# Performance work log

Hardware: AMD Instinct MI355X
Metric: run time of the kernel (lower is better)

## Reference

```python
import jax, jax.numpy as jnp
import numpy as np

N_HEAD = 16
NEG_BIG = 1e10

def setup_inputs() -> dict:
    key = jax.random.key(0)
    k1, k2, k3 = jax.random.split(key, 3)
    B, S, D = 2, 2048, 1024
    x = jax.random.normal(k1, (B, S, D), dtype=jnp.float32)
    c_attn_w = jax.random.normal(k2, (D, 3 * D), dtype=jnp.float32) * 0.02
    c_attn_b = jnp.zeros((3 * D,), dtype=jnp.float32)
    c_proj_w = jax.random.normal(k3, (D, D), dtype=jnp.float32) * 0.02
    c_proj_b = jnp.zeros((D,), dtype=jnp.float32)
    return {"x": x, "c_attn_w": c_attn_w, "c_attn_b": c_attn_b,
            "c_proj_w": c_proj_w, "c_proj_b": c_proj_b}

def reference(x, c_attn_w, c_attn_b, c_proj_w, c_proj_b):
    B, S, D = x.shape
    H = N_HEAD
    hd = D // H
    # Conv1D c_attn: x @ W + b -> (B, S, 3D)
    qkv = x @ c_attn_w + c_attn_b
    q, k, v = jnp.split(qkv, 3, axis=-1)
    # split heads -> (B, H, S, hd)
    q = q.reshape(B, S, H, hd).transpose(0, 2, 1, 3)
    k = k.reshape(B, S, H, hd).transpose(0, 2, 1, 3)
    v = v.reshape(B, S, H, hd).transpose(0, 2, 1, 3)
    # QK^T with scale (scale=True)
    w = jnp.einsum('bhqd,bhkd->bhqk', q, k) / jnp.sqrt(jnp.float32(hd))
    # additive/multiplicative causal mask, exactly as source: w*b - 1e10*(1-b)
    b = jnp.tril(jnp.ones((S, S), dtype=w.dtype))
    w = w * b - NEG_BIG * (1.0 - b)
    w = jax.nn.softmax(w, axis=-1)
    a = jnp.einsum('bhqk,bhkd->bhqd', w, v)
    # merge heads -> (B, S, D)
    a = a.transpose(0, 2, 1, 3).reshape(B, S, D)
    # Conv1D c_proj
    a = a @ c_proj_w + c_proj_b
    # present = stack(key (as (B,H,S,hd)), value)
    present = jnp.stack((k, v))
    return (a, present)
```

## Files before the change

kernel.cpp:

```cpp
#include <hip/hip_runtime.h>
#include <hip/hip_bf16.h>
#include <string.h>

#define BB 2
#define SS 2048
#define DD 1024
#define NH 16
#define TT (BB * SS)
#define N3 (3 * DD)
#define A_SIZE (TT * DD)
#define PRESENT_HALF (BB * NH * SS * 64)
#define C2Q 0.18033688011112043f

typedef __attribute__((ext_vector_type(8))) short short8;
typedef __attribute__((ext_vector_type(4))) float floatx4;
typedef __attribute__((ext_vector_type(8))) unsigned short ushort8;

__device__ __forceinline__ unsigned short f2bf(float f) {
    union { float f; unsigned u; } v; v.f = f;
    unsigned r = v.u + 0x7fffu + ((v.u >> 16) & 1u);
    return (unsigned short)(r >> 16);
}
__device__ __forceinline__ unsigned pack2bf(float a, float b) {
    __hip_bfloat162 h = __float22bfloat162_rn(float2{a, b});
    unsigned u; memcpy(&u, &h, 4); return u;
}
__device__ __forceinline__ float bf2f(unsigned short u) {
    union { unsigned u; float f; } v; v.u = ((unsigned)u) << 16; return v.f;
}

__device__ __forceinline__ void async16(const unsigned short* g, unsigned short* lds) {
    __builtin_amdgcn_global_load_lds(
        (const __attribute__((address_space(1))) unsigned int*)g,
        (__attribute__((address_space(3))) unsigned int*)lds,
        16, 0, 0);
}

__device__ __forceinline__ void transpose_tile(const float* __restrict__ src,
                                               unsigned short* __restrict__ dst,
                                               int R, int C, int bx, int by, int tid) {
    __shared__ float tile[32][33];
    int c0 = bx * 32, r0 = by * 32;
    int tx = tid & 31, ty = tid >> 5;
    for (int i = ty; i < 32; i += 8)
        tile[i][tx] = src[(size_t)(r0 + i) * C + c0 + tx];
    __syncthreads();
    for (int i = ty; i < 32; i += 8)
        dst[(size_t)(c0 + i) * R + r0 + tx] = f2bf(tile[tx][i]);
}

__global__ __launch_bounds__(256)
void prep_kernel(const float* __restrict__ x,
                 const float* __restrict__ wa,
                 const float* __restrict__ wp,
                 unsigned short* __restrict__ xb,
                 unsigned short* __restrict__ wqkvt,
                 unsigned short* __restrict__ wprojt) {
    int bid = blockIdx.x, tid = threadIdx.x;
    if (bid < 2048) {
        int i = (bid * 256 + tid) * 8;
        float4 a = *(const float4*)(x + i);
        float4 b = *(const float4*)(x + i + 4);
        ushort8 o;
        o[0] = f2bf(a.x); o[1] = f2bf(a.y); o[2] = f2bf(a.z); o[3] = f2bf(a.w);
        o[4] = f2bf(b.x); o[5] = f2bf(b.y); o[6] = f2bf(b.z); o[7] = f2bf(b.w);
        *(ushort8*)(xb + i) = o;
    } else if (bid < 2048 + 3072) {
        int b2 = bid - 2048;
        transpose_tile(wa, wqkvt, DD, N3, b2 % 96, b2 / 96, tid);
    } else {
        int b3 = bid - 5120;
        transpose_tile(wp, wprojt, DD, DD, b3 & 31, b3 >> 5, tid);
    }
}

__global__ __launch_bounds__(256)
void kv_aux_kernel(const unsigned short* __restrict__ qkvb,
                   float* __restrict__ out,
                   unsigned short* __restrict__ vT) {
    __shared__ unsigned short tile[64][72];
    const int bh = blockIdx.x, st = blockIdx.y;
    const int b = bh >> 4, h = bh & 15;
    const int tid = threadIdx.x;
    const int r = tid >> 2, c = (tid & 3) * 16;
    const int s = st * 64 + r;

    const unsigned short* kp = qkvb + ((size_t)(b * SS + s)) * 3072 + 1024 + h * 64 + c;
    ushort8 k0 = *(const ushort8*)(kp);
    ushort8 k1 = *(const ushort8*)(kp + 8);
    ushort8 v0 = *(const ushort8*)(kp + 1024);
    ushort8 v1 = *(const ushort8*)(kp + 1032);

    float* pk = out + A_SIZE + (((size_t)(b * NH + h) * SS + s) * 64 + c);
    *(float4*)(pk)      = float4{bf2f(k0[0]), bf2f(k0[1]), bf2f(k0[2]), bf2f(k0[3])};
    *(float4*)(pk + 4)  = float4{bf2f(k0[4]), bf2f(k0[5]), bf2f(k0[6]), bf2f(k0[7])};
    *(float4*)(pk + 8)  = float4{bf2f(k1[0]), bf2f(k1[1]), bf2f(k1[2]), bf2f(k1[3])};
    *(float4*)(pk + 12) = float4{bf2f(k1[4]), bf2f(k1[5]), bf2f(k1[6]), bf2f(k1[7])};
    float* pv = pk + PRESENT_HALF;
    *(float4*)(pv)      = float4{bf2f(v0[0]), bf2f(v0[1]), bf2f(v0[2]), bf2f(v0[3])};
    *(float4*)(pv + 4)  = float4{bf2f(v0[4]), bf2f(v0[5]), bf2f(v0[6]), bf2f(v0[7])};
    *(float4*)(pv + 8)  = float4{bf2f(v1[0]), bf2f(v1[1]), bf2f(v1[2]), bf2f(v1[3])};
    *(float4*)(pv + 12) = float4{bf2f(v1[4]), bf2f(v1[5]), bf2f(v1[6]), bf2f(v1[7])};

    *(ushort8*)(&tile[r][c])     = v0;
    *(ushort8*)(&tile[r][c + 8]) = v1;
    __syncthreads();
    int d = tid >> 2, s0 = (tid & 3) * 16;
    unsigned short tmp[16];
    for (int e = 0; e < 16; ++e) tmp[e] = tile[s0 + e][d];
    unsigned short* dst = vT + ((size_t)bh * 64 + d) * SS + st * 64 + s0;
    *(int4*)(dst)     = *(const int4*)(tmp);
    *(int4*)(dst + 8) = *(const int4*)(tmp + 8);
}

__global__ __launch_bounds__(256)
void gemm1_kernel(const unsigned short* __restrict__ A,
                  const unsigned short* __restrict__ Bt,
                  const float* __restrict__ bias,
                  unsigned short* __restrict__ out_bf) {
    __shared__ unsigned short As[2][128][32];
    __shared__ unsigned short Bs[2][128][32];
    const int tid  = threadIdx.x;
    const int t0   = blockIdx.y * 128;
    const int n0   = blockIdx.x * 128;
    const int wave = tid >> 6, lane = tid & 63;
    const int wm = wave >> 1, wn = wave & 1;
    const int l15 = lane & 15, quad = lane >> 4;
    const int sr = lane >> 2, sc = (lane & 3) * 8;

    floatx4 acc[4][4];
    for (int i = 0; i < 4; ++i)
        for (int j = 0; j < 4; ++j)
            for (int e = 0; e < 4; ++e) acc[i][j][e] = 0.f;

    const unsigned short* gA = A  + (size_t)(t0 + wave * 32 + sr) * 1024 + sc;
    const unsigned short* gB = Bt + (size_t)(n0 + wave * 32 + sr) * 1024 + sc;

    async16(gA,             &As[0][wave * 32][0]);
    async16(gA + 16 * 1024, &As[0][wave * 32 + 16][0]);
    async16(gB,             &Bs[0][wave * 32][0]);
    async16(gB + 16 * 1024, &Bs[0][wave * 32 + 16][0]);

    for (int kt = 0; kt < 32; ++kt) {
        const int cur = kt & 1;
        __syncthreads();
        if (kt < 31) {
            const int k1 = (kt + 1) * 32;
            async16(gA + k1,             &As[cur ^ 1][wave * 32][0]);
            async16(gA + k1 + 16 * 1024, &As[cur ^ 1][wave * 32 + 16][0]);
            async16(gB + k1,             &Bs[cur ^ 1][wave * 32][0]);
            async16(gB + k1 + 16 * 1024, &Bs[cur ^ 1][wave * 32 + 16][0]);
        }
        short8 af[4], bfr[4];
        for (int mt = 0; mt < 4; ++mt)
            af[mt] = *(const short8*)(&As[cur][wm * 64 + mt * 16 + l15][quad * 8]);
        for (int nt = 0; nt < 4; ++nt)
            bfr[nt] = *(const short8*)(&Bs[cur][wn * 64 + nt * 16 + l15][quad * 8]);
        for (int mt = 0; mt < 4; ++mt)
            for (int nt = 0; nt < 4; ++nt)
                acc[mt][nt] = __builtin_amdgcn_mfma_f32_16x16x32_bf16(bfr[nt], af[mt], acc[mt][nt], 0, 0, 0);
    }

    const float qs = (n0 < 1024) ? C2Q : 1.0f;
    for (int mt = 0; mt < 4; ++mt) {
        const int t = t0 + wm * 64 + mt * 16 + l15;
        unsigned short* po = out_bf + (size_t)t * 3072 + n0 + wn * 64;
        for (int nt = 0; nt < 4; ++nt) {
            float4 b4 = *(const float4*)(bias + n0 + wn * 64 + nt * 16 + quad * 4);
            uint2 w = {pack2bf((acc[mt][nt][0] + b4.x) * qs, (acc[mt][nt][1] + b4.y) * qs),
                       pack2bf((acc[mt][nt][2] + b4.z) * qs, (acc[mt][nt][3] + b4.w) * qs)};
            *(uint2*)(po + nt * 16 + quad * 4) = w;
        }
    }
}

__global__ __launch_bounds__(256)
void gemm2_kernel(const unsigned short* __restrict__ A,
                  const unsigned short* __restrict__ Bt,
                  const float* __restrict__ bias,
                  float* __restrict__ out_f) {
    __shared__ unsigned short As[2][128][32];
    __shared__ unsigned short Bs[2][64][32];
    const int tid  = threadIdx.x;
    const int t0   = blockIdx.y * 128;
    const int n0   = blockIdx.x * 64;
    const int wave = tid >> 6, lane = tid & 63;
    const int wm = wave >> 1, wn = wave & 1;
    const int l15 = lane & 15, quad = lane >> 4;
    const int sr = lane >> 2, sc = (lane & 3) * 8;

    floatx4 acc[4][2];
    for (int i = 0; i < 4; ++i)
        for (int j = 0; j < 2; ++j)
            for (int e = 0; e < 4; ++e) acc[i][j][e] = 0.f;

    const unsigned short* gA = A  + (size_t)(t0 + wave * 32 + sr) * 1024 + sc;
    const unsigned short* gB = Bt + (size_t)(n0 + wave * 16 + sr) * 1024 + sc;

    async16(gA,             &As[0][wave * 32][0]);
    async16(gA + 16 * 1024, &As[0][wave * 32 + 16][0]);
    async16(gB,             &Bs[0][wave * 16][0]);

    for (int kt = 0; kt < 32; ++kt) {
        const int cur = kt & 1;
        __syncthreads();
        if (kt < 31) {
            const int k1 = (kt + 1) * 32;
            async16(gA + k1,             &As[cur ^ 1][wave * 32][0]);
            async16(gA + k1 + 16 * 1024, &As[cur ^ 1][wave * 32 + 16][0]);
            async16(gB + k1,             &Bs[cur ^ 1][wave * 16][0]);
        }
        short8 af[4], bfr[2];
        for (int mt = 0; mt < 4; ++mt)
            af[mt] = *(const short8*)(&As[cur][wm * 64 + mt * 16 + l15][quad * 8]);
        for (int nt = 0; nt < 2; ++nt)
            bfr[nt] = *(const short8*)(&Bs[cur][wn * 32 + nt * 16 + l15][quad * 8]);
        for (int mt = 0; mt < 4; ++mt)
            for (int nt = 0; nt < 2; ++nt)
                acc[mt][nt] = __builtin_amdgcn_mfma_f32_16x16x32_bf16(bfr[nt], af[mt], acc[mt][nt], 0, 0, 0);
    }

    for (int mt = 0; mt < 4; ++mt) {
        const int t = t0 + wm * 64 + mt * 16 + l15;
        float* po = out_f + (size_t)t * 1024 + n0 + wn * 32;
        for (int nt = 0; nt < 2; ++nt) {
            float4 b4 = *(const float4*)(bias + n0 + wn * 32 + nt * 16 + quad * 4);
            float4 v = {acc[mt][nt][0] + b4.x, acc[mt][nt][1] + b4.y,
                        acc[mt][nt][2] + b4.z, acc[mt][nt][3] + b4.w};
            *(float4*)(po + nt * 16 + quad * 4) = v;
        }
    }
}

__global__ __launch_bounds__(512)
void flash_kernel(const unsigned short* __restrict__ qkv,
                  const unsigned short* __restrict__ vT,
                  unsigned short* __restrict__ out) {
    __shared__ unsigned short Kt[2][64][72];
    __shared__ unsigned short Vt[2][64][72];
    __shared__ unsigned short Pt[8][16][72];

    const int bh = blockIdx.x;
    const int yy = blockIdx.y;
    const int qy = (yy & 1) ? (yy >> 1) : (15 - (yy >> 1));
    const int b = bh >> 4, h = bh & 15;
    const int tid = threadIdx.x;
    const int wave = tid >> 6, lane = tid & 63;
    const int group = wave >> 2, w4 = wave & 3;
    const int l15 = lane & 15, quad = lane >> 4;

    const int my_qt = 2 * qy + group;
    const int jmax  = 2 * qy + 1;

    const size_t rowb = (size_t)b * SS;

    short8 bq0, bq1;
    {
        const unsigned short* qp = qkv + (rowb + my_qt * 64 + w4 * 16 + l15) * 3072 + h * 64 + quad * 8;
        bq0 = *(const short8*)(qp);
        bq1 = *(const short8*)(qp + 32);
    }

    float l_i = 0.f;
    floatx4 o[4];
    for (int dt = 0; dt < 4; ++dt)
        for (int e = 0; e < 4; ++e) o[dt][e] = 0.f;

    const int qrow_l = w4 * 16 + l15;

    const int rr = tid >> 3, seg = (tid & 7) * 8;
    const unsigned short* kb = qkv + rowb * 3072 + 1024 + h * 64;
    const unsigned short* vb = vT + (size_t)bh * 64 * SS;
    int4 ka, va;

    #define PREF(j) { ka = *(const int4*)(kb + (size_t)((j) * 64 + rr) * 3072 + seg); \
                      va = *(const int4*)(vb + (size_t)rr * SS + (j) * 64 + seg); }
    #define STAGE(bf_) { *(int4*)(&Kt[bf_][rr][seg]) = ka; *(int4*)(&Vt[bf_][rr][seg]) = va; }

    PREF(0);
    STAGE(0);
    if (jmax > 0) PREF(1);

    for (int j = 0; j <= jmax; ++j) {
        const int cur = j & 1;
        __syncthreads();
        if (j < jmax) {
            STAGE(cur ^ 1);
            if (j + 2 <= jmax) PREF(j + 2);
        }
        if (j > my_qt) continue;

        floatx4 sc[4];
        for (int nt = 0; nt < 4; ++nt)
            for (int e = 0; e < 4; ++e) sc[nt][e] = 0.f;
        for (int nt = 0; nt < 4; ++nt) {
            const unsigned short* kp = &Kt[cur][nt * 16 + l15][quad * 8];
            short8 ak0 = *(const short8*)(kp);
            short8 ak1 = *(const short8*)(kp + 32);
            sc[nt] = __builtin_amdgcn_mfma_f32_16x16x32_bf16(ak0, bq0, sc[nt], 0, 0, 0);
            sc[nt] = __builtin_amdgcn_mfma_f32_16x16x32_bf16(ak1, bq1, sc[nt], 0, 0, 0);
        }
        if (j == my_qt) {
            for (int nt = 0; nt < 4; ++nt)
                for (int r = 0; r < 4; ++r)
                    if (nt * 16 + quad * 4 + r > qrow_l) sc[nt][r] = -1.0e30f;
        }

        for (int nt = 0; nt < 4; ++nt)
            for (int r = 0; r < 4; ++r) {
                float p = __builtin_amdgcn_exp2f(sc[nt][r]);
                sc[nt][r] = p;
                l_i += p;
            }

        for (int nt = 0; nt < 4; ++nt) {
            uint2 w = {pack2bf(sc[nt][0], sc[nt][1]), pack2bf(sc[nt][2], sc[nt][3])};
            *(uint2*)(&Pt[wave][l15][nt * 16 + quad * 4]) = w;
        }
        asm volatile("s_waitcnt lgkmcnt(0)" ::: "memory");
        short8 bp0 = *(const short8*)(&Pt[wave][l15][quad * 8]);
        short8 bp1 = *(const short8*)(&Pt[wave][l15][32 + quad * 8]);
        for (int dt = 0; dt < 4; ++dt) {
            const unsigned short* vp = &Vt[cur][dt * 16 + l15][quad * 8];
            short8 av0 = *(const short8*)(vp);
            short8 av1 = *(const short8*)(vp + 32);
            o[dt] = __builtin_amdgcn_mfma_f32_16x16x32_bf16(av0, bp0, o[dt], 0, 0, 0);
            o[dt] = __builtin_amdgcn_mfma_f32_16x16x32_bf16(av1, bp1, o[dt], 0, 0, 0);
        }
    }
    #undef PREF
    #undef STAGE

    l_i += __shfl_xor(l_i, 16);
    l_i += __shfl_xor(l_i, 32);
    float inv = 1.f / l_i;
    const int qrow = my_qt * 64 + w4 * 16 + l15;
    unsigned short* po = out + (rowb + qrow) * 1024 + h * 64;
    for (int dt = 0; dt < 4; ++dt) {
        uint2 w = {pack2bf(o[dt][0] * inv, o[dt][1] * inv),
                   pack2bf(o[dt][2] * inv, o[dt][3] * inv)};
        *(uint2*)(po + dt * 16 + quad * 4) = w;
    }
}

extern "C" void kernel_launch(void* const* d_in, const int* in_sizes, int n_in,
                              void* d_out, int out_size, void* d_ws, size_t ws_size,
                              hipStream_t stream) {
    const float* x        = (const float*)d_in[0];
    const float* c_attn_w = (const float*)d_in[1];
    const float* c_attn_b = (const float*)d_in[2];
    const float* c_proj_w = (const float*)d_in[3];
    const float* c_proj_b = (const float*)d_in[4];
    float* out = (float*)d_out;

    char* ws = (char*)d_ws;
    unsigned short* xb     = (unsigned short*)(ws);
    unsigned short* wqkvt  = (unsigned short*)(ws + 8388608);
    unsigned short* wprojt = (unsigned short*)(ws + 14680064);
    unsigned short* qkvb   = (unsigned short*)(ws + 16777216);
    unsigned short* aout   = (unsigned short*)(ws + 41943040);
    unsigned short* vT     = xb;

    prep_kernel<<<2048 + 3072 + 1024, 256, 0, stream>>>(x, c_attn_w, c_proj_w, xb, wqkvt, wprojt);
    gemm1_kernel<<<dim3(N3 / 128, TT / 128), 256, 0, stream>>>(xb, wqkvt, c_attn_b, qkvb);
    kv_aux_kernel<<<dim3(32, 32), 256, 0, stream>>>(qkvb, out, vT);
    flash_kernel<<<dim3(32, 16), 512, 0, stream>>>(qkvb, vT, aout);
    gemm2_kernel<<<dim3(DD / 64, TT / 128), 256, 0, stream>>>(aout, wprojt, c_proj_b, out);
}
```

Measured before the change: 219.9 us.

## Load K/V fragments directly from global memory in flash attention, drop LDS staging

The flash kernel no longer stages K and V tiles in shared memory with double buffering and block-wide barriers. Each wave now loads its MFMA operand fragments for K and V straight from global memory (relying on L2/cache reuse). The block shrinks from 512 to 256 threads, each block owns one 64-row query tile, and the grid grows to 32x32 with a new balanced tile ordering. This removes __syncthreads and LDS traffic and allows higher occupancy, at the cost of redundant global loads across waves and exposed load latency without prefetch.

```diff
diff --git a/kernel.cpp b/kernel.cpp
--- a/kernel.cpp
+++ b/kernel.cpp
@@ -232,31 +232,26 @@
     }
 }
 
-__global__ __launch_bounds__(512)
+__global__ __launch_bounds__(256, 4)
 void flash_kernel(const unsigned short* __restrict__ qkv,
                   const unsigned short* __restrict__ vT,
                   unsigned short* __restrict__ out) {
-    __shared__ unsigned short Kt[2][64][72];
-    __shared__ unsigned short Vt[2][64][72];
-    __shared__ unsigned short Pt[8][16][72];
+    __shared__ unsigned short Pt[4][16][72];
 
     const int bh = blockIdx.x;
-    const int yy = blockIdx.y;
-    const int qy = (yy & 1) ? (yy >> 1) : (15 - (yy >> 1));
+    const int y  = blockIdx.y;
+    const int qq = y >> 3, cc = y & 7;
+    const int qt = (qq == 0) ? cc : (qq == 1) ? 15 - cc : (qq == 2) ? 16 + cc : 31 - cc;
     const int b = bh >> 4, h = bh & 15;
     const int tid = threadIdx.x;
     const int wave = tid >> 6, lane = tid & 63;
-    const int group = wave >> 2, w4 = wave & 3;
     const int l15 = lane & 15, quad = lane >> 4;
-
-    const int my_qt = 2 * qy + group;
-    const int jmax  = 2 * qy + 1;
 
     const size_t rowb = (size_t)b * SS;
 
     short8 bq0, bq1;
     {
-        const unsigned short* qp = qkv + (rowb + my_qt * 64 + w4 * 16 + l15) * 3072 + h * 64 + quad * 8;
+        const unsigned short* qp = qkv + (rowb + qt * 64 + wave * 16 + l15) * 3072 + h * 64 + quad * 8;
         bq0 = *(const short8*)(qp);
         bq1 = *(const short8*)(qp + 32);
     }
@@ -266,41 +261,36 @@
     for (int dt = 0; dt < 4; ++dt)
         for (int e = 0; e < 4; ++e) o[dt][e] = 0.f;
 
-    const int qrow_l = w4 * 16 + l15;
-
-    const int rr = tid >> 3, seg = (tid & 7) * 8;
-    const unsigned short* kb = qkv + rowb * 3072 + 1024 + h * 64;
-    const unsigned short* vb = vT + (size_t)bh * 64 * SS;
-    int4 ka, va;
-
-    #define PREF(j) { ka = *(const int4*)(kb + (size_t)((j) * 64 + rr) * 3072 + seg); \
-                      va = *(const int4*)(vb + (size_t)rr * SS + (j) * 64 + seg); }
-    #define STAGE(bf_) { *(int4*)(&Kt[bf_][rr][seg]) = ka; *(int4*)(&Vt[bf_][rr][seg]) = va; }
-
-    PREF(0);
-    STAGE(0);
-    if (jmax > 0) PREF(1);
-
-    for (int j = 0; j <= jmax; ++j) {
-        const int cur = j & 1;
-        __syncthreads();
-        if (j < jmax) {
-            STAGE(cur ^ 1);
-            if (j + 2 <= jmax) PREF(j + 2);
-        }
-        if (j > my_qt) continue;
-
+    const int qrow_l = wave * 16 + l15;
+
+    const unsigned short* kb = qkv + (rowb + l15) * 3072 + 1024 + h * 64 + quad * 8;
+    const unsigned short* vb = vT + ((size_t)bh * 64 + l15) * SS + quad * 8;
+
+    for (int j = 0; j <= qt; ++j) {
+        short8 ak[4][2];
+        const unsigned short* kj = kb + (size_t)j * 64 * 3072;
+        for (int nt = 0; nt < 4; ++nt) {
+            const unsigned short* kp = kj + (size_t)nt * 16 * 3072;
+            ak[nt][0] = *(const short8*)(kp);
+            ak[nt][1] = *(const short8*)(kp + 32);
+        }
         floatx4 sc[4];
         for (int nt = 0; nt < 4; ++nt)
             for (int e = 0; e < 4; ++e) sc[nt][e] = 0.f;
         for (int nt = 0; nt < 4; ++nt) {
-            const unsigned short* kp = &Kt[cur][nt * 16 + l15][quad * 8];
-            short8 ak0 = *(const short8*)(kp);
-            short8 ak1 = *(const short8*)(kp + 32);
-            sc[nt] = __builtin_amdgcn_mfma_f32_16x16x32_bf16(ak0, bq0, sc[nt], 0, 0, 0);
-            sc[nt] = __builtin_amdgcn_mfma_f32_16x16x32_bf16(ak1, bq1, sc[nt], 0, 0, 0);
-        }
-        if (j == my_qt) {
+            sc[nt] = __builtin_amdgcn_mfma_f32_16x16x32_bf16(ak[nt][0], bq0, sc[nt], 0, 0, 0);
+            sc[nt] = __builtin_amdgcn_mfma_f32_16x16x32_bf16(ak[nt][1], bq1, sc[nt], 0, 0, 0);
+        }
+
+        short8 av[4][2];
+        const unsigned short* vj = vb + j * 64;
+        for (int dt = 0; dt < 4; ++dt) {
+            const unsigned short* vp = vj + (size_t)dt * 16 * SS;
+            av[dt][0] = *(const short8*)(vp);
+            av[dt][1] = *(const short8*)(vp + 32);
+        }
+
+        if (j == qt) {
             for (int nt = 0; nt < 4; ++nt)
                 for (int r = 0; r < 4; ++r)
                     if (nt * 16 + quad * 4 + r > qrow_l) sc[nt][r] = -1.0e30f;
@@ -321,20 +311,15 @@
         short8 bp0 = *(const short8*)(&Pt[wave][l15][quad * 8]);
         short8 bp1 = *(const short8*)(&Pt[wave][l15][32 + quad * 8]);
         for (int dt = 0; dt < 4; ++dt) {
-            const unsigned short* vp = &Vt[cur][dt * 16 + l15][quad * 8];
-            short8 av0 = *(const short8*)(vp);
-            short8 av1 = *(const short8*)(vp + 32);
-            o[dt] = __builtin_amdgcn_mfma_f32_16x16x32_bf16(av0, bp0, o[dt], 0, 0, 0);
-            o[dt] = __builtin_amdgcn_mfma_f32_16x16x32_bf16(av1, bp1, o[dt], 0, 0, 0);
-        }
-    }
-    #undef PREF
-    #undef STAGE
+            o[dt] = __builtin_amdgcn_mfma_f32_16x16x32_bf16(av[dt][0], bp0, o[dt], 0, 0, 0);
+            o[dt] = __builtin_amdgcn_mfma_f32_16x16x32_bf16(av[dt][1], bp1, o[dt], 0, 0, 0);
+        }
+    }
 
     l_i += __shfl_xor(l_i, 16);
     l_i += __shfl_xor(l_i, 32);
     float inv = 1.f / l_i;
-    const int qrow = my_qt * 64 + w4 * 16 + l15;
+    const int qrow = qt * 64 + wave * 16 + l15;
     unsigned short* po = out + (rowb + qrow) * 1024 + h * 64;
     for (int dt = 0; dt < 4; ++dt) {
         uint2 w = {pack2bf(o[dt][0] * inv, o[dt][1] * inv),
@@ -364,6 +349,6 @@
     prep_kernel<<<2048 + 3072 + 1024, 256, 0, stream>>>(x, c_attn_w, c_proj_w, xb, wqkvt, wprojt);
     gemm1_kernel<<<dim3(N3 / 128, TT / 128), 256, 0, stream>>>(xb, wqkvt, c_attn_b, qkvb);
     kv_aux_kernel<<<dim3(32, 32), 256, 0, stream>>>(qkvb, out, vT);
-    flash_kernel<<<dim3(32, 16), 512, 0, stream>>>(qkvb, vT, aout);
+    flash_kernel<<<dim3(32, 32), 256, 0, stream>>>(qkvb, vT, aout);
     gemm2_kernel<<<dim3(DD / 64, TT / 128), 256, 0, stream>>>(aout, wprojt, c_proj_b, out);
 }
```

Measured after the change: 290.7 us. 32.2% more time.
